# Kernel optimization log

Hardware: AMD Instinct MI355X
Metric: run time of the kernel (lower is better)

The kernel has to match this reference:

```python
import math
import jax, jax.numpy as jnp
import numpy as np

DIM = 256
B, S = 4, 4096

def setup_inputs() -> dict:
    key = jax.random.key(0)
    k1, k2, k3, k4 = jax.random.split(key, 4)
    x = jax.random.normal(k1, (B, S, DIM), dtype=jnp.float32)
    W = jax.random.normal(k2, (3 * DIM, DIM), dtype=jnp.float32) * 0.02
    b = jax.random.normal(k3, (3 * DIM,), dtype=jnp.float32) * 0.02
    attention_mask = jax.random.randint(k4, (B, 1, S), 0, 2, dtype=jnp.int32)
    return {"x": x, "W": W, "b": b, "attention_mask": attention_mask}

def reference(x, W, b, attention_mask):
    # qkv projection: Linear(dim, 3*dim) -> x @ W^T + b
    qkv = jnp.einsum("bsd,ed->bse", x, W) + b  # [B,S,3*DIM]
    q, k, v = jnp.split(qkv, 3, axis=-1)
    # NOTE: module computes q @ v^T (not q @ k^T) -- faithful to source
    scores = jnp.einsum("bqd,bkd->bqk", q, v) / math.sqrt(DIM)  # [B,S,S]
    scores = jnp.where(attention_mask == 0, -jnp.inf, scores)
    attn = jax.nn.softmax(scores, axis=-1)
    # dropout in eval mode -> identity
    out = jnp.einsum("bqk,bkd->bqd", attn, v)  # [B,S,DIM]
    return out
```

## Files before the change

kernel.cpp:

```cpp
#include <hip/hip_runtime.h>
#include <hip/hip_bf16.h>

#define DIMC 256
#define NB 4
#define NS 4096
#define KT 32

typedef __attribute__((ext_vector_type(4))) float f32x4;
typedef __attribute__((ext_vector_type(8))) short bf16x8;

__device__ __forceinline__ ushort f2bf(float f) {
  __hip_bfloat16 h = __float2bfloat16(f);
  return *reinterpret_cast<ushort*>(&h);
}
__device__ __forceinline__ float bf2f(ushort h) {
  uint u = ((uint)h) << 16;
  float f;
  __builtin_memcpy(&f, &u, 4);
  return f;
}

__device__ __forceinline__ void gload16(const ushort* g, ushort* l) {
  __builtin_amdgcn_global_load_lds(
      (const __attribute__((address_space(1))) unsigned int*)g,
      (__attribute__((address_space(3))) unsigned int*)l,
      16, 0, 0);
}

__global__ __launch_bounds__(256) void prep_kernel(
    const float* __restrict__ W, const int* __restrict__ mask,
    ushort* __restrict__ Whl, uint* __restrict__ pm32)
{
  if (blockIdx.x < 512) {
    const int col = blockIdx.x;
    const int k = threadIdx.x;
    const int srcrow = (col < 256) ? col : (col + 256);
    float f = W[(size_t)srcrow * 256 + k];
    ushort h = f2bf(f);
    Whl[(size_t)col * 256 + k] = h;
    Whl[131072 + (size_t)col * 256 + k] = f2bf(f - bf2f(h));
  } else {
    int t = (blockIdx.x - 512) * 256 + threadIdx.x;
    int b = t >> 7;
    int kt = (t >> 1) & 63;
    int kh = t & 1;
    const int* mrow = mask + b * NS + kt * 64 + kh * 32;
    uint wd = 0;
    for (int g = 0; g < 4; ++g)
      for (int ntl = 0; ntl < 2; ++ntl)
        for (int r = 0; r < 4; ++r)
          if (mrow[ntl * 16 + 4 * g + r] != 0) wd |= 1u << (8 * g + ntl * 4 + r);
    pm32[t] = wd;
  }
}

__global__ __launch_bounds__(256) void qv_proj_kernel(
    const float* __restrict__ x, const ushort* __restrict__ Whl,
    const float* __restrict__ bias,
    ushort* __restrict__ qb, ushort* __restrict__ vb, ushort* __restrict__ vtb)
{
  const int tid  = threadIdx.x;
  const int w    = tid >> 6;
  const int lane = tid & 63;
  const int l15  = lane & 15;
  const int g    = (lane >> 4) & 3;
  const int r0   = blockIdx.x << 6;
  const int colbase = w << 7;

  __shared__ ushort olds[64 * 520];

  f32x4 acc[4][8];
  #pragma unroll
  for (int rt = 0; rt < 4; ++rt)
    #pragma unroll
    for (int ct = 0; ct < 8; ++ct) { acc[rt][ct].x=0.f; acc[rt][ct].y=0.f; acc[rt][ct].z=0.f; acc[rt][ct].w=0.f; }

  #pragma unroll 1
  for (int st = 0; st < 8; ++st) {
    bf16x8 xh[4], xl[4];
    #pragma unroll
    for (int rt = 0; rt < 4; ++rt) {
      const float* p = x + (size_t)(r0 + rt * 16 + l15) * DIMC + st * 32 + g * 8;
      float4 f0 = *(const float4*)p;
      float4 f1 = *(const float4*)(p + 4);
      union { bf16x8 v; ushort u[8]; } uh, ul;
      #pragma unroll
      for (int e = 0; e < 8; ++e) {
        float fe = (e < 4) ? ((const float*)&f0)[e] : ((const float*)&f1)[e - 4];
        ushort h = f2bf(fe);
        uh.u[e] = h;
        ul.u[e] = f2bf(fe - bf2f(h));
      }
      xh[rt] = uh.v;
      xl[rt] = ul.v;
    }
    #pragma unroll
    for (int ct = 0; ct < 8; ++ct) {
      const ushort* wp = Whl + (size_t)(colbase + ct * 16 + l15) * 256 + st * 32 + g * 8;
      bf16x8 wh = *(const bf16x8*)wp;
      bf16x8 wl = *(const bf16x8*)(wp + 131072);
      #pragma unroll
      for (int rt = 0; rt < 4; ++rt) {
        acc[rt][ct] = __builtin_amdgcn_mfma_f32_16x16x32_bf16(xh[rt], wh, acc[rt][ct], 0, 0, 0);
        acc[rt][ct] = __builtin_amdgcn_mfma_f32_16x16x32_bf16(xl[rt], wh, acc[rt][ct], 0, 0, 0);
        acc[rt][ct] = __builtin_amdgcn_mfma_f32_16x16x32_bf16(xh[rt], wl, acc[rt][ct], 0, 0, 0);
      }
    }
  }

  const float qscale = (colbase < 256) ? 0.0625f : 1.0f;
  #pragma unroll
  for (int ct = 0; ct < 8; ++ct) {
    const int col = colbase + ct * 16 + l15;
    const float bv = bias[(col < 256) ? col : (col + 256)];
    #pragma unroll
    for (int rt = 0; rt < 4; ++rt) {
      #pragma unroll
      for (int r = 0; r < 4; ++r)
        olds[(rt * 16 + 4 * g + r) * 520 + col] = f2bf((acc[rt][ct][r] + bv) * qscale);
    }
  }
  __syncthreads();

  #pragma unroll
  for (int i = 0; i < 16; ++i) {
    int task = tid + i * 256;
    int row = task >> 6, ch = task & 63;
    uint4 d = *(const uint4*)&olds[row * 520 + ch * 8];
    if (ch < 32) *(uint4*)&qb[(size_t)(r0 + row) * DIMC + ch * 8] = d;
    else         *(uint4*)&vb[(size_t)(r0 + row) * DIMC + (ch - 32) * 8] = d;
  }
  const int bbp = r0 >> 12;
  const int s0  = r0 & (NS - 1);
  const int vcol = tid;
  #pragma unroll
  for (int o = 0; o < 8; ++o) {
    union { uint4 v; ushort u[8]; } pk;
    #pragma unroll
    for (int j = 0; j < 8; ++j)
      pk.u[j] = olds[(o * 8 + j) * 520 + 256 + vcol];
    *(uint4*)&vtb[((size_t)(bbp * DIMC + vcol)) * NS + s0 + o * 8] = pk.v;
  }
}

__global__ __launch_bounds__(256, 2) void attn_kernel(
    const ushort* __restrict__ qb, const ushort* __restrict__ vb,
    const ushort* __restrict__ vtb, const uint* __restrict__ pm32,
    float* __restrict__ outA, float* __restrict__ opB,
    float* __restrict__ mlA, float* __restrict__ mlB)
{
  const int tid  = threadIdx.x;
  const int w    = tid >> 6;
  const int lane = tid & 63;
  const int l15  = lane & 15;
  const int g    = (lane >> 4) & 3;
  const int kh   = w & 1;
  const int pq   = w >> 1;

  const int s     = blockIdx.x & 1;
  const int qb64  = blockIdx.x >> 1;
  const int qrow0 = qb64 << 6;
  const int bb    = qrow0 >> 12;
  const int koff  = s << 11;

  float* opart = s ? opB : outA;
  float* mlp   = s ? mlB : mlA;

  extern __shared__ __align__(16) char smem[];
  uint*   pmlds = (uint*)smem;
  ushort* vs0  = (ushort*)(smem + 1024);
  ushort* vs1  = vs0 + KT * DIMC;
  ushort* vt0  = vs1 + KT * DIMC;
  ushort* vt1  = vt0 + KT * DIMC;
  ushort* psb  = vt1 + KT * DIMC;
  float*  lx   = (float*)(psb + 2 * 32 * 40);

  bf16x8 qreg[2][8];
  #pragma unroll
  for (int qt = 0; qt < 2; ++qt) {
    const int qrow = qrow0 + (pq << 5) + (qt << 4) + l15;
    #pragma unroll
    for (int st = 0; st < 8; ++st)
      qreg[qt][st] = *(const bf16x8*)&qb[(size_t)qrow * DIMC + ((st * 4 + g) << 3)];
  }

  if (tid < 128) pmlds[tid] = pm32[(bb << 7) + tid];

  auto stage_vs = [&](int kt, ushort* vsN) {
    const ushort* vbase = vb + ((size_t)(bb * NS + koff + kt * KT)) * DIMC;
    #pragma unroll
    for (int i = 0; i < 4; ++i) {
      int rr0 = (w << 3) + (i << 1);
      int row = rr0 + (lane >> 5);
      int cs  = lane & 31;
      gload16(vbase + row * DIMC + ((cs ^ (row & 7)) << 3), vsN + (rr0 << 8));
    }
  };
  auto stage_vt = [&](int kt, ushort* vtN) {
    #pragma unroll
    for (int i = 0; i < 4; ++i) {
      int d0 = i << 6;
      int dim = (d0 + lane) ^ ((w & 3) << 1);
      gload16(vtb + ((size_t)(bb * DIMC + dim)) * NS + koff + kt * KT + (w << 3),
              vtN + ((w << 8) + d0) * 8);
    }
  };

  stage_vs(0, vs0);
  stage_vt(0, vt0);
  asm volatile("s_waitcnt vmcnt(0)" ::: "memory");
  __syncthreads();

  f32x4 acc_o[2][8];
  #pragma unroll
  for (int qt = 0; qt < 2; ++qt)
    #pragma unroll
    for (int nt = 0; nt < 8; ++nt) { acc_o[qt][nt].x=0.f; acc_o[qt][nt].y=0.f; acc_o[qt][nt].z=0.f; acc_o[qt][nt].w=0.f; }
  float l_s[2] = {0.f, 0.f};

  ushort* psw = psb + pq * (32 * 40);

  #pragma unroll 1
  for (int t = 0; t < 64; ++t) {
    ushort* vsQ = (t & 1) ? vs1 : vs0;
    ushort* vtP = (t & 1) ? vt1 : vt0;
    ushort* vsS = (t & 1) ? vs0 : vs1;
    ushort* vtS = (t & 1) ? vt0 : vt1;

    if (t + 1 < 64) { stage_vs(t + 1, vsS); stage_vt(t + 1, vtS); }

    f32x4 sacc[2];
    sacc[0].x=0.f; sacc[0].y=0.f; sacc[0].z=0.f; sacc[0].w=0.f;
    sacc[1] = sacc[0];
    __builtin_amdgcn_s_setprio(1);
    #pragma unroll
    for (int st = 0; st < 8; ++st) {
      const int key = (kh << 4) + l15;
      bf16x8 af = *(const bf16x8*)&vsQ[(key * 32 + ((st * 4 + g) ^ (key & 7))) * 8];
      sacc[0] = __builtin_amdgcn_mfma_f32_16x16x32_bf16(af, qreg[0][st], sacc[0], 0, 0, 0);
      sacc[1] = __builtin_amdgcn_mfma_f32_16x16x32_bf16(af, qreg[1][st], sacc[1], 0, 0, 0);
    }
    __builtin_amdgcn_s_setprio(0);

    const int ktg6 = (s << 5) + (t >> 1);
    uint mybits = (pmlds[(ktg6 << 1) + (t & 1)] >> ((g << 3) + (kh << 2))) & 0xfu;
    #pragma unroll
    for (int qt = 0; qt < 2; ++qt) {
      float p[4];
      #pragma unroll
      for (int r = 0; r < 4; ++r) {
        float vv = (mybits & (1u << r)) ? sacc[qt][r] : -1e30f;
        p[r] = __expf(vv);
      }
      float rs = (p[0] + p[1]) + (p[2] + p[3]);
      rs += __shfl_xor(rs, 16);
      rs += __shfl_xor(rs, 32);
      l_s[qt] += rs;
      uint2 pk;
      pk.x = (uint)f2bf(p[0]) | ((uint)f2bf(p[1]) << 16);
      pk.y = (uint)f2bf(p[2]) | ((uint)f2bf(p[3]) << 16);
      *(uint2*)&psw[((qt << 4) + l15) * 40 + (kh << 4) + (g << 2)] = pk;
    }

    asm volatile("s_waitcnt lgkmcnt(0)" ::: "memory");
    __builtin_amdgcn_sched_barrier(0);
    __builtin_amdgcn_s_barrier();
    __builtin_amdgcn_sched_barrier(0);

    bf16x8 pa0 = *(const bf16x8*)&psw[l15 * 40 + (g << 3)];
    bf16x8 pa1 = *(const bf16x8*)&psw[(16 + l15) * 40 + (g << 3)];
    __builtin_amdgcn_s_setprio(1);
    #pragma unroll
    for (int ntl = 0; ntl < 8; ++ntl) {
      const int d = ((kh << 3) + ntl) * 16 + l15;
      bf16x8 vf = *(const bf16x8*)&vtP[((g << 8) + (d ^ (g << 1))) * 8];
      acc_o[0][ntl] = __builtin_amdgcn_mfma_f32_16x16x32_bf16(vf, pa0, acc_o[0][ntl], 0, 0, 0);
      acc_o[1][ntl] = __builtin_amdgcn_mfma_f32_16x16x32_bf16(vf, pa1, acc_o[1][ntl], 0, 0, 0);
    }
    __builtin_amdgcn_s_setprio(0);

    asm volatile("s_waitcnt vmcnt(0) lgkmcnt(0)" ::: "memory");
    __builtin_amdgcn_sched_barrier(0);
    __builtin_amdgcn_s_barrier();
    __builtin_amdgcn_sched_barrier(0);
  }

  if (kh) {
    if (g == 0) {
      lx[(pq << 5) + l15]      = l_s[0];
      lx[(pq << 5) + 16 + l15] = l_s[1];
    }
  }
  __syncthreads();
  #pragma unroll
  for (int qt = 0; qt < 2; ++qt) {
    const int qrow = qrow0 + (pq << 5) + (qt << 4) + l15;
    const size_t obase = (size_t)qrow * DIMC + (kh << 7) + 4 * g;
    #pragma unroll
    for (int ntl = 0; ntl < 8; ++ntl) {
      f32x4 o = acc_o[qt][ntl];
      *(float4*)&opart[obase + ntl * 16] = *(float4*)&o;
    }
    if (!kh && g == 0)
      mlp[qrow] = l_s[qt] + lx[(pq << 5) + (qt << 4) + l15];
  }
}

__global__ __launch_bounds__(256) void merge_kernel(
    float* __restrict__ outA, const float* __restrict__ opB,
    const float* __restrict__ mlA, const float* __restrict__ mlB)
{
  int id = blockIdx.x * 256 + threadIdx.x;
  int row = id >> 6;
  int c = (id & 63) << 2;
  float inv = 1.f / (mlA[row] + mlB[row]);
  size_t o = (size_t)row * DIMC + c;
  float4 a = *(const float4*)&outA[o];
  float4 b = *(const float4*)&opB[o];
  float4 r;
  r.x = (a.x + b.x) * inv;
  r.y = (a.y + b.y) * inv;
  r.z = (a.z + b.z) * inv;
  r.w = (a.w + b.w) * inv;
  *(float4*)&outA[o] = r;
}

extern "C" void kernel_launch(void* const* d_in, const int* in_sizes, int n_in,
                              void* d_out, int out_size, void* d_ws, size_t ws_size,
                              hipStream_t stream) {
  const float* x    = (const float*)d_in[0];
  const float* W    = (const float*)d_in[1];
  const float* bias = (const float*)d_in[2];
  const int*   mask = (const int*)d_in[3];
  float* out = (float*)d_out;

  const size_t n = (size_t)NB * NS * DIMC;
  ushort* qb  = (ushort*)d_ws;
  ushort* vb  = qb + n;
  ushort* vtb = vb + n;
  uint* pm32 = (uint*)(vtb + n);
  ushort* Whl = (ushort*)(pm32 + 512);
  float* opB = (float*)(Whl + 262144);
  float* mlA = opB + n;
  float* mlB = mlA + (NB * NS);

  prep_kernel<<<514, 256, 0, stream>>>(W, mask, Whl, pm32);
  qv_proj_kernel<<<(NB * NS) / 64, 256, 0, stream>>>(x, Whl, bias, qb, vb, vtb);

  const int smem_bytes = 1024 + 4 * (KT * DIMC) * 2 + 2 * 32 * 40 * 2 + 256;
  attn_kernel<<<512, 256, smem_bytes, stream>>>(qb, vb, vtb, pm32, out, opB, mlA, mlB);
  merge_kernel<<<(NB * NS * DIMC / 4) / 256, 256, 0, stream>>>(out, opB, mlA, mlB);
}
```

Baseline: 152.9 us.

## Use 512-thread blocks with software-pipelined PV against next QK tile

Doubles the threads per attention block so that each warp owns 16 query rows instead of 32, which halves the per-thread register state for Q and the output accumulators. The loop is restructured so the P·V MFMAs for the previous tile run right after the QK MFMAs of the current tile. The V^T tile is now staged one iteration later and the wait uses a partial vmcnt, letting loads overlap compute. Row sums are written per key-half and combined in the merge kernel, which removes the shared-memory reduction. The costs are more barrier traffic from more warps and subtler hazards in the waitcnt accounting.

```diff
diff --git a/kernel.cpp b/kernel.cpp
--- a/kernel.cpp
+++ b/kernel.cpp
@@ -143,7 +143,7 @@
   }
 }
 
-__global__ __launch_bounds__(256, 2) void attn_kernel(
+__global__ __launch_bounds__(512, 4) void attn_kernel(
     const ushort* __restrict__ qb, const ushort* __restrict__ vb,
     const ushort* __restrict__ vtb, const uint* __restrict__ pm32,
     float* __restrict__ outA, float* __restrict__ opB,
@@ -173,24 +173,20 @@
   ushort* vt0  = vs1 + KT * DIMC;
   ushort* vt1  = vt0 + KT * DIMC;
   ushort* psb  = vt1 + KT * DIMC;
-  float*  lx   = (float*)(psb + 2 * 32 * 40);
-
-  bf16x8 qreg[2][8];
-  #pragma unroll
-  for (int qt = 0; qt < 2; ++qt) {
-    const int qrow = qrow0 + (pq << 5) + (qt << 4) + l15;
-    #pragma unroll
-    for (int st = 0; st < 8; ++st)
-      qreg[qt][st] = *(const bf16x8*)&qb[(size_t)qrow * DIMC + ((st * 4 + g) << 3)];
-  }
+
+  const int qrow_w = qrow0 + (pq << 4) + l15;
+  bf16x8 qreg[8];
+  #pragma unroll
+  for (int st = 0; st < 8; ++st)
+    qreg[st] = *(const bf16x8*)&qb[(size_t)qrow_w * DIMC + ((st * 4 + g) << 3)];
 
   if (tid < 128) pmlds[tid] = pm32[(bb << 7) + tid];
 
   auto stage_vs = [&](int kt, ushort* vsN) {
     const ushort* vbase = vb + ((size_t)(bb * NS + koff + kt * KT)) * DIMC;
     #pragma unroll
-    for (int i = 0; i < 4; ++i) {
-      int rr0 = (w << 3) + (i << 1);
+    for (int i = 0; i < 2; ++i) {
+      int rr0 = (w << 2) + (i << 1);
       int row = rr0 + (lane >> 5);
       int cs  = lane & 31;
       gload16(vbase + row * DIMC + ((cs ^ (row & 7)) << 3), vsN + (rr0 << 8));
@@ -198,111 +194,118 @@
   };
   auto stage_vt = [&](int kt, ushort* vtN) {
     #pragma unroll
-    for (int i = 0; i < 4; ++i) {
-      int d0 = i << 6;
-      int dim = (d0 + lane) ^ ((w & 3) << 1);
-      gload16(vtb + ((size_t)(bb * DIMC + dim)) * NS + koff + kt * KT + (w << 3),
-              vtN + ((w << 8) + d0) * 8);
+    for (int i = 0; i < 2; ++i) {
+      int cstart = (w << 7) + (i << 6);
+      int kc = cstart >> 8;
+      int dim = ((cstart & 255) + lane) ^ (kc << 1);
+      gload16(vtb + ((size_t)(bb * DIMC + dim)) * NS + koff + kt * KT + (kc << 3),
+              vtN + cstart * 8);
     }
   };
 
   stage_vs(0, vs0);
-  stage_vt(0, vt0);
-  asm volatile("s_waitcnt vmcnt(0)" ::: "memory");
   __syncthreads();
 
-  f32x4 acc_o[2][8];
-  #pragma unroll
-  for (int qt = 0; qt < 2; ++qt)
-    #pragma unroll
-    for (int nt = 0; nt < 8; ++nt) { acc_o[qt][nt].x=0.f; acc_o[qt][nt].y=0.f; acc_o[qt][nt].z=0.f; acc_o[qt][nt].w=0.f; }
-  float l_s[2] = {0.f, 0.f};
-
-  ushort* psw = psb + pq * (32 * 40);
+  f32x4 acc_o[8];
+  #pragma unroll
+  for (int nt = 0; nt < 8; ++nt) { acc_o[nt].x=0.f; acc_o[nt].y=0.f; acc_o[nt].z=0.f; acc_o[nt].w=0.f; }
+  float l_s = 0.f;
+
+  ushort* psw = psb + pq * (16 * 40);
 
   #pragma unroll 1
   for (int t = 0; t < 64; ++t) {
     ushort* vsQ = (t & 1) ? vs1 : vs0;
-    ushort* vtP = (t & 1) ? vt1 : vt0;
     ushort* vsS = (t & 1) ? vs0 : vs1;
-    ushort* vtS = (t & 1) ? vt0 : vt1;
-
-    if (t + 1 < 64) { stage_vs(t + 1, vsS); stage_vt(t + 1, vtS); }
-
-    f32x4 sacc[2];
-    sacc[0].x=0.f; sacc[0].y=0.f; sacc[0].z=0.f; sacc[0].w=0.f;
-    sacc[1] = sacc[0];
+    ushort* vtS = (t & 1) ? vt1 : vt0;
+    ushort* vtP = (t & 1) ? vt0 : vt1;
+
+    if (t + 1 < 64) stage_vs(t + 1, vsS);
+    stage_vt(t, vtS);
+
+    f32x4 sacc;
+    sacc.x=0.f; sacc.y=0.f; sacc.z=0.f; sacc.w=0.f;
     __builtin_amdgcn_s_setprio(1);
     #pragma unroll
     for (int st = 0; st < 8; ++st) {
       const int key = (kh << 4) + l15;
       bf16x8 af = *(const bf16x8*)&vsQ[(key * 32 + ((st * 4 + g) ^ (key & 7))) * 8];
-      sacc[0] = __builtin_amdgcn_mfma_f32_16x16x32_bf16(af, qreg[0][st], sacc[0], 0, 0, 0);
-      sacc[1] = __builtin_amdgcn_mfma_f32_16x16x32_bf16(af, qreg[1][st], sacc[1], 0, 0, 0);
+      sacc = __builtin_amdgcn_mfma_f32_16x16x32_bf16(af, qreg[st], sacc, 0, 0, 0);
     }
     __builtin_amdgcn_s_setprio(0);
+
+    if (t > 0) {
+      bf16x8 pa = *(const bf16x8*)&psw[l15 * 40 + (g << 3)];
+      __builtin_amdgcn_s_setprio(1);
+      #pragma unroll
+      for (int ntl = 0; ntl < 8; ++ntl) {
+        const int d = ((kh << 3) + ntl) * 16 + l15;
+        bf16x8 vf = *(const bf16x8*)&vtP[((g << 8) + (d ^ (g << 1))) * 8];
+        acc_o[ntl] = __builtin_amdgcn_mfma_f32_16x16x32_bf16(vf, pa, acc_o[ntl], 0, 0, 0);
+      }
+      __builtin_amdgcn_s_setprio(0);
+    }
 
     const int ktg6 = (s << 5) + (t >> 1);
     uint mybits = (pmlds[(ktg6 << 1) + (t & 1)] >> ((g << 3) + (kh << 2))) & 0xfu;
-    #pragma unroll
-    for (int qt = 0; qt < 2; ++qt) {
-      float p[4];
-      #pragma unroll
-      for (int r = 0; r < 4; ++r) {
-        float vv = (mybits & (1u << r)) ? sacc[qt][r] : -1e30f;
-        p[r] = __expf(vv);
-      }
-      float rs = (p[0] + p[1]) + (p[2] + p[3]);
-      rs += __shfl_xor(rs, 16);
-      rs += __shfl_xor(rs, 32);
-      l_s[qt] += rs;
-      uint2 pk;
-      pk.x = (uint)f2bf(p[0]) | ((uint)f2bf(p[1]) << 16);
-      pk.y = (uint)f2bf(p[2]) | ((uint)f2bf(p[3]) << 16);
-      *(uint2*)&psw[((qt << 4) + l15) * 40 + (kh << 4) + (g << 2)] = pk;
-    }
+    float pv[4];
+    #pragma unroll
+    for (int r = 0; r < 4; ++r) {
+      float vv = (mybits & (1u << r)) ? sacc[r] : -1e30f;
+      pv[r] = __expf(vv);
+    }
+    float rs = (pv[0] + pv[1]) + (pv[2] + pv[3]);
+    rs += __shfl_xor(rs, 16);
+    rs += __shfl_xor(rs, 32);
+    l_s += rs;
 
     asm volatile("s_waitcnt lgkmcnt(0)" ::: "memory");
     __builtin_amdgcn_sched_barrier(0);
     __builtin_amdgcn_s_barrier();
     __builtin_amdgcn_sched_barrier(0);
 
-    bf16x8 pa0 = *(const bf16x8*)&psw[l15 * 40 + (g << 3)];
-    bf16x8 pa1 = *(const bf16x8*)&psw[(16 + l15) * 40 + (g << 3)];
+    {
+      uint2 pk;
+      pk.x = (uint)f2bf(pv[0]) | ((uint)f2bf(pv[1]) << 16);
+      pk.y = (uint)f2bf(pv[2]) | ((uint)f2bf(pv[3]) << 16);
+      *(uint2*)&psw[l15 * 40 + (kh << 4) + (g << 2)] = pk;
+    }
+
+    if (t + 1 < 64)
+      asm volatile("s_waitcnt vmcnt(4) lgkmcnt(0)" ::: "memory");
+    else
+      asm volatile("s_waitcnt vmcnt(2) lgkmcnt(0)" ::: "memory");
+    __builtin_amdgcn_sched_barrier(0);
+    __builtin_amdgcn_s_barrier();
+    __builtin_amdgcn_sched_barrier(0);
+  }
+
+  asm volatile("s_waitcnt vmcnt(0)" ::: "memory");
+  __builtin_amdgcn_sched_barrier(0);
+  __builtin_amdgcn_s_barrier();
+  __builtin_amdgcn_sched_barrier(0);
+  {
+    ushort* vtP = vt1;
+    bf16x8 pa = *(const bf16x8*)&psw[l15 * 40 + (g << 3)];
     __builtin_amdgcn_s_setprio(1);
     #pragma unroll
     for (int ntl = 0; ntl < 8; ++ntl) {
       const int d = ((kh << 3) + ntl) * 16 + l15;
       bf16x8 vf = *(const bf16x8*)&vtP[((g << 8) + (d ^ (g << 1))) * 8];
-      acc_o[0][ntl] = __builtin_amdgcn_mfma_f32_16x16x32_bf16(vf, pa0, acc_o[0][ntl], 0, 0, 0);
-      acc_o[1][ntl] = __builtin_amdgcn_mfma_f32_16x16x32_bf16(vf, pa1, acc_o[1][ntl], 0, 0, 0);
+      acc_o[ntl] = __builtin_amdgcn_mfma_f32_16x16x32_bf16(vf, pa, acc_o[ntl], 0, 0, 0);
     }
     __builtin_amdgcn_s_setprio(0);
-
-    asm volatile("s_waitcnt vmcnt(0) lgkmcnt(0)" ::: "memory");
-    __builtin_amdgcn_sched_barrier(0);
-    __builtin_amdgcn_s_barrier();
-    __builtin_amdgcn_sched_barrier(0);
-  }
-
-  if (kh) {
-    if (g == 0) {
-      lx[(pq << 5) + l15]      = l_s[0];
-      lx[(pq << 5) + 16 + l15] = l_s[1];
-    }
-  }
-  __syncthreads();
-  #pragma unroll
-  for (int qt = 0; qt < 2; ++qt) {
-    const int qrow = qrow0 + (pq << 5) + (qt << 4) + l15;
-    const size_t obase = (size_t)qrow * DIMC + (kh << 7) + 4 * g;
+  }
+
+  {
+    const int qrow = qrow_w;
+    const size_t obase = (size_t)qrow * DIMC + 4 * g;
     #pragma unroll
     for (int ntl = 0; ntl < 8; ++ntl) {
-      f32x4 o = acc_o[qt][ntl];
-      *(float4*)&opart[obase + ntl * 16] = *(float4*)&o;
-    }
-    if (!kh && g == 0)
-      mlp[qrow] = l_s[qt] + lx[(pq << 5) + (qt << 4) + l15];
+      f32x4 o = acc_o[ntl];
+      *(float4*)&opart[obase + ((kh << 3) + ntl) * 16] = *(float4*)&o;
+    }
+    if (g == 0) mlp[(size_t)qrow * 2 + kh] = l_s;
   }
 }
 
@@ -313,7 +316,9 @@
   int id = blockIdx.x * 256 + threadIdx.x;
   int row = id >> 6;
   int c = (id & 63) << 2;
-  float inv = 1.f / (mlA[row] + mlB[row]);
+  float lT = (mlA[(size_t)row * 2] + mlA[(size_t)row * 2 + 1]) +
+             (mlB[(size_t)row * 2] + mlB[(size_t)row * 2 + 1]);
+  float inv = 1.f / lT;
   size_t o = (size_t)row * DIMC + c;
   float4 a = *(const float4*)&outA[o];
   float4 b = *(const float4*)&opB[o];
@@ -342,12 +347,12 @@
   ushort* Whl = (ushort*)(pm32 + 512);
   float* opB = (float*)(Whl + 262144);
   float* mlA = opB + n;
-  float* mlB = mlA + (NB * NS);
+  float* mlB = mlA + 2 * (NB * NS);
 
   prep_kernel<<<514, 256, 0, stream>>>(W, mask, Whl, pm32);
   qv_proj_kernel<<<(NB * NS) / 64, 256, 0, stream>>>(x, Whl, bias, qb, vb, vtb);
 
-  const int smem_bytes = 1024 + 4 * (KT * DIMC) * 2 + 2 * 32 * 40 * 2 + 256;
-  attn_kernel<<<512, 256, smem_bytes, stream>>>(qb, vb, vtb, pm32, out, opB, mlA, mlB);
+  const int smem_bytes = 1024 + 4 * (KT * DIMC) * 2 + 4 * 16 * 40 * 2;
+  attn_kernel<<<512, 512, smem_bytes, stream>>>(qb, vb, vtb, pm32, out, opB, mlA, mlB);
   merge_kernel<<<(NB * NS * DIMC / 4) / 256, 256, 0, stream>>>(out, opB, mlA, mlB);
 }
```

Result: slower. 163.9 us (+7.2%).
